# Optimization experiments

Measured on AMD Instinct MI355X. Metric: run time of the kernel, lower is better.

The kernel has to match this reference:

```python
import jax, jax.numpy as jnp
import numpy as np

N = 50000
NEG_SLOPE = 0.01  # F.leaky_relu default


def gcn_conv(x, edge_index, edge_weight, W, b):
    """PyG GCNConv: h = x @ W; symmetric-normalized aggregation with self-loops; + bias."""
    n = x.shape[0]
    h = x @ W                                # [N, out]
    src, dst = edge_index[0], edge_index[1]
    # degree includes self-loop weight 1.0 per node
    deg = jax.ops.segment_sum(edge_weight, dst, num_segments=n) + 1.0
    dinv = jax.lax.rsqrt(deg)                # deg >= 1, no zero guard needed
    norm = dinv[src] * edge_weight * dinv[dst]
    agg = jax.ops.segment_sum(norm[:, None] * h[src], dst, num_segments=n)
    agg = agg + (dinv * dinv)[:, None] * h   # self-loop contribution: deg^-1 * h_i
    return agg + b


def setup_inputs() -> dict:
    key = jax.random.key(0)
    ks = jax.random.split(key, 24)
    in_size, hid, out = 256, 64, 32
    E = 800000
    d = {}
    for i, nm in enumerate(["x1", "x2", "x3"]):
        d[nm] = jax.random.normal(ks[i], (N, in_size), dtype=jnp.float32)
    for i, nm in enumerate(["edge_index1", "edge_index2", "edge_index3"]):
        d[nm] = jax.random.randint(ks[3 + i], (2, E), 0, N, dtype=jnp.int32)
    for i, nm in enumerate(["edge_weight1", "edge_weight2", "edge_weight3"]):
        d[nm] = jax.random.uniform(ks[6 + i], (E,), dtype=jnp.float32)
    s_in = 1.0 / np.sqrt(in_size)
    s_h = 1.0 / np.sqrt(hid)
    for i, nm in enumerate(["W1", "W2", "W3"]):
        d[nm] = jax.random.uniform(ks[9 + i], (in_size, hid), minval=-s_in, maxval=s_in, dtype=jnp.float32)
    for i, nm in enumerate(["b1", "b2", "b3"]):
        d[nm] = jax.random.uniform(ks[12 + i], (hid,), minval=-s_in, maxval=s_in, dtype=jnp.float32)
    d["fc_w"] = jax.random.uniform(ks[15], (hid, 1), minval=-s_h, maxval=s_h, dtype=jnp.float32)
    d["fc_b"] = jax.random.uniform(ks[16], (1,), minval=-s_h, maxval=s_h, dtype=jnp.float32)
    for i, nm in enumerate(["W11", "W22", "W33"]):
        d[nm] = jax.random.uniform(ks[17 + i], (hid, out), minval=-s_h, maxval=s_h, dtype=jnp.float32)
    for i, nm in enumerate(["b11", "b22", "b33"]):
        d[nm] = jax.random.uniform(ks[20 + i], (out,), minval=-s_h, maxval=s_h, dtype=jnp.float32)
    return d


def reference(x1, x2, x3, edge_index1, edge_index2, edge_index3,
              edge_weight1, edge_weight2, edge_weight3,
              W1, W2, W3, b1, b2, b3, fc_w, fc_b,
              W11, W22, W33, b11, b22, b33):
    # branch embeddings (dropout is identity in eval mode)
    e1 = jax.nn.relu(gcn_conv(x1, edge_index1, edge_weight1, W1, b1))
    e2 = jax.nn.relu(gcn_conv(x2, edge_index2, edge_weight2, W2, b2))
    e3 = jax.nn.relu(gcn_conv(x3, edge_index3, edge_weight3, W3, b3))
    # attention coefficients
    c1 = jnp.exp(jax.nn.leaky_relu(e1 @ fc_w + fc_b, NEG_SLOPE))  # [N,1]
    c2 = jnp.exp(jax.nn.leaky_relu(e2 @ fc_w + fc_b, NEG_SLOPE))
    c3 = jnp.exp(jax.nn.leaky_relu(e3 @ fc_w + fc_b, NEG_SLOPE))
    cd = c1 + c2 + c3
    coef1, coef2, coef3 = c1 / cd, c2 / cd, c3 / cd
    combined = e1 * coef1 + e2 * coef2 + e3 * coef3
    out1 = gcn_conv(combined, edge_index1, edge_weight1, W11, b11)
    out2 = gcn_conv(combined, edge_index2, edge_weight2, W22, b22)
    out3 = gcn_conv(combined, edge_index3, edge_weight3, W33, b33)
    return (out1 + out2 + out3, coef1, coef2, coef3)
```

## Files before the change

kernel.cpp:

```cpp
#include <hip/hip_runtime.h>
#include <hip/hip_fp16.h>
#include <math.h>

#define NN    50000
#define INF_  256
#define HID   64
#define OUTF  32
#define EE    800000
#define TOTN  (3 * NN)
#define NBKT  196
#define NBIN  (3 * NBKT)
#define CBLK  392
#define NCNT  (3 * CBLK)
#define GB    782
#define NGEMM (3 * GB)
#define MAXB  5120
#define NBLK  12500

typedef unsigned long long u64;
typedef unsigned int       u32;
typedef unsigned short     u16;
typedef _Float16           f16;
typedef f16   f16x8 __attribute__((ext_vector_type(8)));
typedef f16   f16x4 __attribute__((ext_vector_type(4)));
typedef float f32x4 __attribute__((ext_vector_type(4)));

__global__ __launch_bounds__(256) void k_prep(
        const float* __restrict__ W1, const float* __restrict__ W2, const float* __restrict__ W3,
        f16* __restrict__ Wt2, u32* __restrict__ bin_total) {
    int blk = blockIdx.x, t = threadIdx.x;
    if (blk == 3) {
        for (int i = t; i < NBIN; i += 256) bin_total[i] = 0;
        return;
    }
    const float* W = (blk == 0) ? W1 : (blk == 1) ? W2 : W3;
    f16* wt = Wt2 + blk * 16384;
    for (int idx = t; idx < 16384; idx += 256) {
        int e    = idx & 7;
        int lane = (idx >> 3) & 63;
        int kt   = (idx >> 9) & 7;
        int c    = idx >> 12;
        int col  = c * 16 + (lane & 15);
        int k    = kt * 32 + ((lane >> 4) << 3) + e;
        wt[idx] = (f16)W[k * HID + col];
    }
}

__global__ __launch_bounds__(256) void k_count(
        const int* __restrict__ ei1, const int* __restrict__ ei2, const int* __restrict__ ei3,
        u32* __restrict__ bin_total, u32* __restrict__ blockbase) {
    __shared__ u32 bins[NBKT];
    int cb  = blockIdx.x;
    int br  = cb / CBLK;
    int blk = cb - br * CBLK;
    const int* ei = (br == 0) ? ei1 : (br == 1) ? ei2 : ei3;
    int t = threadIdx.x;
    for (int i = t; i < NBKT; i += 256) bins[i] = 0;
    __syncthreads();
    int e0 = blk * 2048;
#pragma unroll
    for (int k = 0; k < 8; ++k) {
        int e = e0 + k * 256 + t;
        if (e < EE) atomicAdd(&bins[(u32)ei[EE + e] >> 8], 1u);
    }
    __syncthreads();
    for (int i = t; i < NBKT; i += 256) {
        u32 c = bins[i];
        u32 base = atomicAdd(&bin_total[br * NBKT + i], c);
        blockbase[cb * NBKT + i] = base;
    }
}

__global__ __launch_bounds__(256) void k_scan(const u32* __restrict__ bin_total,
                                              u32* __restrict__ binstart) {
    __shared__ u32 s[256];
    int t = threadIdx.x;
    u32 c[3]; u32 sum = 0;
#pragma unroll
    for (int k = 0; k < 3; ++k) {
        int i = t * 3 + k;
        c[k] = (i < NBIN) ? bin_total[i] : 0;
        sum += c[k];
    }
    s[t] = sum;
    __syncthreads();
    for (int d = 1; d < 256; d <<= 1) {
        u32 v = (t >= d) ? s[t - d] : 0;
        __syncthreads();
        s[t] += v;
        __syncthreads();
    }
    u32 run = s[t] - sum;
#pragma unroll
    for (int k = 0; k < 3; ++k) {
        int i = t * 3 + k;
        if (i < NBIN) binstart[i] = run;
        run += c[k];
    }
    if (t == 255) binstart[NBIN] = run;
}

__global__ __launch_bounds__(256) void k_scatgemm(
        const int* __restrict__ ei1, const int* __restrict__ ei2, const int* __restrict__ ei3,
        const float* __restrict__ ew1, const float* __restrict__ ew2, const float* __restrict__ ew3,
        const u32* __restrict__ binstart, const u32* __restrict__ blockbase,
        u64* __restrict__ bucketed,
        const float* __restrict__ x1, const float* __restrict__ x2, const float* __restrict__ x3,
        const f16* __restrict__ Wt2, __half* __restrict__ h) {
    __shared__ f16 xl[64][264];
    int bid = blockIdx.x;
    int q = bid / 3, r = bid - q * 3;
    int t = threadIdx.x;

    if (r == 2) {
        u32* cur = (u32*)xl;
        int cb  = q;
        int br  = cb / CBLK;
        int blk = cb - br * CBLK;
        const int*   ei = (br == 0) ? ei1 : (br == 1) ? ei2 : ei3;
        const float* ew = (br == 0) ? ew1 : (br == 1) ? ew2 : ew3;
        for (int i = t; i < NBKT; i += 256) cur[i] = 0;
        __syncthreads();
        int e0 = blk * 2048;
#pragma unroll
        for (int k = 0; k < 8; ++k) {
            int e = e0 + k * 256 + t;
            if (e < EE) {
                u32 dst = (u32)ei[EE + e];
                u32 src = (u32)ei[e];
                u32 bkt = dst >> 8;
                u32 rnk = atomicAdd(&cur[bkt], 1u);
                u32 pos = binstart[br * NBKT + bkt] + blockbase[cb * NBKT + bkt] + rnk;
                bucketed[pos] = ((u64)__float_as_uint(ew[e]) << 32) | (src << 8) | (dst & 0xffu);
            }
        }
        return;
    }

    int gid = q * 2 + r;
    if (gid >= NGEMM) return;
    int b = gid / GB;
    int row_base = (gid - b * GB) * 64;
    const float4* x4 = reinterpret_cast<const float4*>((b == 0) ? x1 : (b == 1) ? x2 : x3);
    const f16* wt2 = Wt2 + b * 16384;
    __half* hb = h + (size_t)b * NN * HID;

    float4 v[16];
#pragma unroll
    for (int j = 0; j < 16; ++j) {
        int flat = j * 256 + t;
        int gr = row_base + (flat >> 6);
        v[j] = (gr < NN) ? x4[(size_t)row_base * 64 + flat]
                         : make_float4(0.f, 0.f, 0.f, 0.f);
    }
#pragma unroll
    for (int j = 0; j < 16; ++j) {
        int flat = j * 256 + t;
        int rr = flat >> 6, c4 = flat & 63;
        f16x4 p = {(f16)v[j].x, (f16)v[j].y, (f16)v[j].z, (f16)v[j].w};
        *(f16x4*)&xl[rr][c4 * 4] = p;
    }
    __syncthreads();

    int w    = t >> 6;
    int lane = t & 63;
    int lrow = lane & 15;
    int lk   = (lane >> 4) * 8;
    int arow = (w << 4) + lrow;

    f32x4 acc[4] = {{0,0,0,0},{0,0,0,0},{0,0,0,0},{0,0,0,0}};
#pragma unroll
    for (int kt = 0; kt < 8; ++kt) {
        f16x8 af = *(const f16x8*)&xl[arow][kt * 32 + lk];
#pragma unroll
        for (int c = 0; c < 4; ++c) {
            f16x8 bf = *(const f16x8*)&wt2[((c * 8 + kt) * 64 + lane) * 8];
            acc[c] = __builtin_amdgcn_mfma_f32_16x16x32_f16(af, bf, acc[c], 0, 0, 0);
        }
    }
    int orow0 = row_base + (w << 4) + ((lane >> 4) << 2);
#pragma unroll
    for (int c = 0; c < 4; ++c) {
#pragma unroll
        for (int i = 0; i < 4; ++i) {
            int row = orow0 + i;
            if (row < NN) hb[(size_t)row * HID + c * 16 + lrow] = __float2half(acc[c][i]);
        }
    }
}

__global__ __launch_bounds__(256) void k_bucket(
        const u64* __restrict__ bucketed, const u32* __restrict__ bin_total,
        const u32* __restrict__ binstart,
        u32* __restrict__ nodeinfo, float* __restrict__ dinv,
        u32* __restrict__ csr, __half* __restrict__ h) {
    __shared__ u32   scnt[256];
    __shared__ float swsum[256];
    __shared__ u32   scur[256];
    __shared__ u32   sscan[256];
    __shared__ float sdiv[256];
    __shared__ u32   lcsr[MAXB];
    int bin = blockIdx.x;
    int br  = bin / NBKT;
    int bkt = bin - br * NBKT;
    int t = threadIdx.x;
    u32 base = binstart[bin];
    u32 ecnt = bin_total[bin];
    scnt[t] = 0; swsum[t] = 0.f; scur[t] = 0;
    __syncthreads();
    for (u32 i = t; i < ecnt; i += 256) {
        u64 e = bucketed[base + i];
        u32 dl = (u32)e & 0xffu;
        atomicAdd(&scnt[dl], 1u);
        atomicAdd(&swsum[dl], __uint_as_float((u32)(e >> 32)));
    }
    __syncthreads();
    sscan[t] = scnt[t];
    __syncthreads();
    for (int d = 1; d < 256; d <<= 1) {
        u32 v = (t >= d) ? sscan[t - d] : 0;
        __syncthreads();
        sscan[t] += v;
        __syncthreads();
    }
    u32 lstart = sscan[t] - scnt[t];
    float d = rsqrtf(1.0f + swsum[t]);
    sdiv[t] = d;
    int n = bkt * 256 + t;
    if (n < NN) {
        int gi = br * NN + n;
        nodeinfo[gi] = ((base + lstart) << 10) | scnt[t];
        dinv[gi]     = d;
    }
    __syncthreads();
    for (u32 i = t; i < ecnt; i += 256) {
        u64 e = bucketed[base + i];
        u32 dl  = (u32)e & 0xffu;
        u32 src = (u32)(e >> 8) & 0xffffu;
        float w = __uint_as_float((u32)(e >> 32));
        u32 rnk = atomicAdd(&scur[dl], 1u);
        u32 ls  = sscan[dl] - scnt[dl];
        lcsr[ls + rnk] = ((u32)__half_as_ushort(__float2half(w)) << 16) | src;
    }
    __syncthreads();
    for (u32 i = t; i < ecnt; i += 256) csr[base + i] = lcsr[i];

    int nrows = NN - bkt * 256; if (nrows > 256) nrows = 256;
    u32* hrow = (u32*)(h + ((size_t)br * NN + (size_t)bkt * 256) * HID);
    for (int i = t; i < nrows * 32; i += 256) {
        float dd = sdiv[i >> 5];
        __half2 hv = *(__half2*)&hrow[i];
        float2 v = __half22float2(hv);
        __half2 r = __float22half2_rn(make_float2(v.x * dd, v.y * dd));
        hrow[i] = *(u32*)&r;
    }
}

__global__ __launch_bounds__(256) void k_agg1(
        const u32* __restrict__ csr, const u32* __restrict__ nodeinfo,
        const float* __restrict__ dinv,
        const float* __restrict__ b1, const float* __restrict__ b2, const float* __restrict__ b3,
        const __half* __restrict__ h, __half* __restrict__ e) {
    int bid = blockIdx.x;
    int br  = bid / NBLK;
    int nb  = bid - br * NBLK;
    int t   = threadIdx.x;
    int f2  = t & 31;
    int eo  = (t >> 5) & 1;
    int sub = __builtin_amdgcn_readfirstlane(t >> 6);
    int n   = nb * 4 + sub;

    const float* bi = (br == 0) ? b1 : (br == 1) ? b2 : b3;
    const __half2* hb2 = (const __half2*)(h + (size_t)br * NN * HID);
    int i   = br * NN + n;
    u32 inf = nodeinfo[i];
    int cc  = (int)(inf & 1023u);
    int st  = (int)(inf >> 10);
    float d = dinv[i];
    float2 hs = __half22float2(hb2[(size_t)n * 32 + f2]);

    float ax = 0.f, ay = 0.f;
    int cm1 = cc - 1;
    for (int j = 0; j < cc; j += 16) {
        u32 ee[8]; __half2 vv[8];
#pragma unroll
        for (int u = 0; u < 8; ++u) {
            int jj = j + 2 * u + eo;
            ee[u] = csr[st + (jj < cm1 ? jj : cm1)];
            if (jj >= cc) ee[u] &= 0xffffu;
        }
#pragma unroll
        for (int u = 0; u < 8; ++u)
            vv[u] = hb2[(size_t)(ee[u] & 0xffff) * 32 + f2];
#pragma unroll
        for (int u = 0; u < 8; ++u) {
            float w = __half2float(__ushort_as_half((u16)(ee[u] >> 16)));
            float2 v = __half22float2(vv[u]);
            ax = fmaf(w, v.x, ax);
            ay = fmaf(w, v.y, ay);
        }
    }
    ax += __shfl_xor(ax, 32);
    ay += __shfl_xor(ay, 32);
    float2 bv = ((const float2*)bi)[f2];
    float ex = fmaxf(bv.x + d * (hs.x + ax), 0.f);
    float ey = fmaxf(bv.y + d * (hs.y + ay), 0.f);
    if (eo == 0)
        ((__half2*)e)[((size_t)br * NN + n) * 32 + f2] = __float22half2_rn(make_float2(ex, ey));
}

__global__ __launch_bounds__(256) void k_attn(
        const __half* __restrict__ e,
        const float* __restrict__ fc_w, const float* __restrict__ fc_b,
        __half* __restrict__ comb, float* __restrict__ coef_out) {
    int t    = threadIdx.x;
    int lane = t & 63;
    int sub  = __builtin_amdgcn_readfirstlane(t >> 6);
    int half = lane >> 5;
    int f2   = lane & 31;
    int n    = blockIdx.x * 8 + sub * 2 + half;
    float2 wv = ((const float2*)fc_w)[f2];
    float fb = fc_b[0];
    const __half2* e2 = (const __half2*)e;

    float2 ev[3]; float c[3];
#pragma unroll
    for (int b = 0; b < 3; ++b) {
        ev[b] = __half22float2(e2[((size_t)b * NN + n) * 32 + f2]);
        float dd = ev[b].x * wv.x + ev[b].y * wv.y;
#pragma unroll
        for (int off = 16; off > 0; off >>= 1) dd += __shfl_xor(dd, off);
        float z = dd + fb;
        z = (z > 0.f) ? z : 0.01f * z;
        c[b] = expf(z);
    }
    float cd = c[0] + c[1] + c[2];
    float coef0 = c[0] / cd, coef1 = c[1] / cd, coef2 = c[2] / cd;
    float cx = ev[0].x * coef0 + ev[1].x * coef1 + ev[2].x * coef2;
    float cy = ev[0].y * coef0 + ev[1].y * coef1 + ev[2].y * coef2;
    ((__half2*)comb)[(size_t)n * 32 + f2] = __float22half2_rn(make_float2(cx, cy));
    if (f2 == 0) {
        coef_out[n]          = coef0;
        coef_out[NN + n]     = coef1;
        coef_out[2 * NN + n] = coef2;
    }
}

__global__ __launch_bounds__(256) void k_gemm2(
        const __half* __restrict__ comb,
        const float* __restrict__ W11, const float* __restrict__ W22, const float* __restrict__ W33,
        const float* __restrict__ dinv, __half* __restrict__ h2) {
    __shared__ float Wls[3][HID][OUTF];
    __shared__ __half cl[8][HID];
    int t = threadIdx.x;
    {
        const float4* w40 = reinterpret_cast<const float4*>(W11);
        const float4* w41 = reinterpret_cast<const float4*>(W22);
        const float4* w42 = reinterpret_cast<const float4*>(W33);
        float4* d0 = reinterpret_cast<float4*>(&Wls[0][0][0]);
        float4* d1 = reinterpret_cast<float4*>(&Wls[1][0][0]);
        float4* d2 = reinterpret_cast<float4*>(&Wls[2][0][0]);
#pragma unroll
        for (int j = 0; j < 2; ++j) {
            d0[t + j * 256] = w40[t + j * 256];
            d1[t + j * 256] = w41[t + j * 256];
            d2[t + j * 256] = w42[t + j * 256];
        }
    }
    int row0 = blockIdx.x * 8;
    ((u32*)cl)[t] = ((const u32*)(comb + (size_t)row0 * HID))[t];
    __syncthreads();

    int col = t & 31;
    int rr  = t >> 5;
    int row = row0 + rr;
    float a0 = 0.f, a1 = 0.f, a2 = 0.f;
    for (int k = 0; k < HID; ++k) {
        float cv = __half2float(cl[rr][k]);
        a0 = fmaf(cv, Wls[0][k][col], a0);
        a1 = fmaf(cv, Wls[1][k][col], a1);
        a2 = fmaf(cv, Wls[2][k][col], a2);
    }
    float d0 = dinv[row], d1 = dinv[NN + row], d2 = dinv[2 * NN + row];
    h2[(size_t)0 * NN * OUTF + (size_t)row * OUTF + col] = __float2half(a0 * d0);
    h2[(size_t)1 * NN * OUTF + (size_t)row * OUTF + col] = __float2half(a1 * d1);
    h2[(size_t)2 * NN * OUTF + (size_t)row * OUTF + col] = __float2half(a2 * d2);
}

__global__ __launch_bounds__(256) void k_agg2p(
        const u32* __restrict__ csr, const u32* __restrict__ nodeinfo,
        const float* __restrict__ dinv,
        const __half* __restrict__ h2, float* __restrict__ outp) {
    int bid = blockIdx.x;
    int br  = bid / NBLK;
    int nb  = bid - br * NBLK;
    int t   = threadIdx.x;
    int f2  = t & 15;
    int eo  = (t >> 4) & 3;
    int sub = __builtin_amdgcn_readfirstlane(t >> 6);
    int n   = nb * 4 + sub;

    int i   = br * NN + n;
    u32 inf = nodeinfo[i];
    int cc  = (int)(inf & 1023u);
    int st  = (int)(inf >> 10);
    const __half2* h2b = (const __half2*)(h2 + (size_t)br * NN * OUTF);
    float ax = 0.f, ay = 0.f;
    int cm1 = cc - 1;
    for (int j = 0; j < cc; j += 16) {
        u32 ee[4]; __half2 vv[4];
#pragma unroll
        for (int u = 0; u < 4; ++u) {
            int jj = j + 4 * u + eo;
            ee[u] = csr[st + (jj < cm1 ? jj : cm1)];
            if (jj >= cc) ee[u] &= 0xffffu;
        }
#pragma unroll
        for (int u = 0; u < 4; ++u)
            vv[u] = h2b[(size_t)(ee[u] & 0xffff) * 16 + f2];
#pragma unroll
        for (int u = 0; u < 4; ++u) {
            float w = __half2float(__ushort_as_half((u16)(ee[u] >> 16)));
            float2 v = __half22float2(vv[u]);
            ax = fmaf(w, v.x, ax);
            ay = fmaf(w, v.y, ay);
        }
    }
    ax += __shfl_xor(ax, 16); ay += __shfl_xor(ay, 16);
    ax += __shfl_xor(ax, 32); ay += __shfl_xor(ay, 32);
    float d = dinv[i];
    float2 hs = __half22float2(h2b[(size_t)n * 16 + f2]);
    if (eo == 0)
        ((float2*)outp)[((size_t)br * NN + n) * 16 + f2] =
            make_float2(d * (ax + hs.x), d * (ay + hs.y));
}

__global__ __launch_bounds__(256) void k_sum(
        const float* __restrict__ outp,
        const float* __restrict__ b11, const float* __restrict__ b22, const float* __restrict__ b33,
        float* __restrict__ out) {
    int i = blockIdx.x * 256 + threadIdx.x;
    int f2 = i & 15;
    const float2* p = (const float2*)outp;
    float2 v0 = p[i];
    float2 v1 = p[(size_t)NN * 16 + i];
    float2 v2 = p[(size_t)2 * NN * 16 + i];
    float2 bA = ((const float2*)b11)[f2];
    float2 bB = ((const float2*)b22)[f2];
    float2 bC = ((const float2*)b33)[f2];
    ((float2*)out)[i] = make_float2(v0.x + v1.x + v2.x + bA.x + bB.x + bC.x,
                                    v0.y + v1.y + v2.y + bA.y + bB.y + bC.y);
}

extern "C" void kernel_launch(void* const* d_in, const int* in_sizes, int n_in,
                              void* d_out, int out_size, void* d_ws, size_t ws_size,
                              hipStream_t stream) {
    const float* x1  = (const float*)d_in[0];
    const float* x2  = (const float*)d_in[1];
    const float* x3  = (const float*)d_in[2];
    const int*   ei1 = (const int*)d_in[3];
    const int*   ei2 = (const int*)d_in[4];
    const int*   ei3 = (const int*)d_in[5];
    const float* ew1 = (const float*)d_in[6];
    const float* ew2 = (const float*)d_in[7];
    const float* ew3 = (const float*)d_in[8];
    const float* W1  = (const float*)d_in[9];
    const float* W2  = (const float*)d_in[10];
    const float* W3  = (const float*)d_in[11];
    const float* b1  = (const float*)d_in[12];
    const float* b2  = (const float*)d_in[13];
    const float* b3  = (const float*)d_in[14];
    const float* fcw = (const float*)d_in[15];
    const float* fcb = (const float*)d_in[16];
    const float* W11 = (const float*)d_in[17];
    const float* W22 = (const float*)d_in[18];
    const float* W33 = (const float*)d_in[19];
    const float* b11 = (const float*)d_in[20];
    const float* b22 = (const float*)d_in[21];
    const float* b33 = (const float*)d_in[22];

    float* out = (float*)d_out;
    float* coef_out = out + (size_t)NN * OUTF;

    u64*   bucketed  = (u64*)d_ws;
    float* outp      = (float*)d_ws;
    u32*   csr       = (u32*)(bucketed + 3 * EE);
    u32*   bin_total = csr + 3 * EE;
    u32*   binstart  = bin_total + NBIN;
    u32*   blockbase = binstart + NBIN + 4;
    float* dinv      = (float*)(blockbase + NCNT * NBKT);
    u32*   nodeinfo  = (u32*)(dinv + TOTN);
    f16*   Wt2       = (f16*)(nodeinfo + TOTN);
    __half* h        = (__half*)(Wt2 + 3 * 16384);
    __half* comb     = h + (size_t)TOTN * HID;
    __half* h2       = comb + (size_t)NN * HID;
    __half* e        = h2 + (size_t)TOTN * OUTF;

    k_prep<<<dim3(4), 256, 0, stream>>>(W1, W2, W3, Wt2, bin_total);
    k_count<<<dim3(NCNT), 256, 0, stream>>>(ei1, ei2, ei3, bin_total, blockbase);
    k_scan<<<dim3(1), 256, 0, stream>>>(bin_total, binstart);
    k_scatgemm<<<dim3(NCNT * 3), 256, 0, stream>>>(ei1, ei2, ei3, ew1, ew2, ew3,
                                                   binstart, blockbase, bucketed,
                                                   x1, x2, x3, Wt2, h);
    k_bucket<<<dim3(NBIN), 256, 0, stream>>>(bucketed, bin_total, binstart,
                                             nodeinfo, dinv, csr, h);

    k_agg1<<<dim3(3 * NBLK), 256, 0, stream>>>(csr, nodeinfo, dinv, b1, b2, b3, h, e);
    k_attn<<<dim3(NN / 8), 256, 0, stream>>>(e, fcw, fcb, comb, coef_out);
    k_gemm2<<<dim3(NN / 8), 256, 0, stream>>>(comb, W11, W22, W33, dinv, h2);
    k_agg2p<<<dim3(3 * NBLK), 256, 0, stream>>>(csr, nodeinfo, dinv, h2, outp);
    k_sum<<<dim3(3125), 256, 0, stream>>>(outp, b11, b22, b33, out);
}
```

Baseline: 286.5 us.

## Stage edge scatter in shared memory for coalesced bucketed writes, larger edge chunks

The edge-scatter blocks now first count and prefix-scan destination buckets locally, place each edge into a shared-memory staging array sorted by bucket, and then write that array to global memory in contiguous runs instead of doing random 8-byte scattered stores. Edge chunks grow from 2048 to 4096 per block, which halves the count/scatter block count, and the kernel's block mix changes to four GEMM blocks per scatter block. Edge weights are converted to fp16 at scatter time, so the bucket kernel no longer converts them. The cost is an extra pass over edge indices, a 256-step shared scan, and a larger shared footprint that may reduce occupancy.

```diff
diff --git a/kernel.cpp b/kernel.cpp
--- a/kernel.cpp
+++ b/kernel.cpp
@@ -10,7 +10,7 @@
 #define TOTN  (3 * NN)
 #define NBKT  196
 #define NBIN  (3 * NBKT)
-#define CBLK  392
+#define CBLK  196
 #define NCNT  (3 * CBLK)
 #define GB    782
 #define NGEMM (3 * GB)
@@ -20,6 +20,7 @@
 typedef unsigned long long u64;
 typedef unsigned int       u32;
 typedef unsigned short     u16;
+typedef unsigned char      u8;
 typedef _Float16           f16;
 typedef f16   f16x8 __attribute__((ext_vector_type(8)));
 typedef f16   f16x4 __attribute__((ext_vector_type(4)));
@@ -57,9 +58,9 @@
     int t = threadIdx.x;
     for (int i = t; i < NBKT; i += 256) bins[i] = 0;
     __syncthreads();
-    int e0 = blk * 2048;
-#pragma unroll
-    for (int k = 0; k < 8; ++k) {
+    int e0 = blk * 4096;
+#pragma unroll
+    for (int k = 0; k < 16; ++k) {
         int e = e0 + k * 256 + t;
         if (e < EE) atomicAdd(&bins[(u32)ei[EE + e] >> 8], 1u);
     }
@@ -107,38 +108,70 @@
         u64* __restrict__ bucketed,
         const float* __restrict__ x1, const float* __restrict__ x2, const float* __restrict__ x3,
         const f16* __restrict__ Wt2, __half* __restrict__ h) {
-    __shared__ f16 xl[64][264];
+    __shared__ __align__(16) char smem[36864];
     int bid = blockIdx.x;
-    int q = bid / 3, r = bid - q * 3;
+    int q = bid / 5, r = bid - q * 5;
     int t = threadIdx.x;
 
-    if (r == 2) {
-        u32* cur = (u32*)xl;
+    if (r == 4) {
+        u64* ent  = (u64*)smem;
+        u32* acnt = (u32*)(smem + 32768);
+        u32* ascn = acnt + 256;
+        u32* acur = ascn + 256;
+        u32* adel = acur + 256;
         int cb  = q;
         int br  = cb / CBLK;
         int blk = cb - br * CBLK;
         const int*   ei = (br == 0) ? ei1 : (br == 1) ? ei2 : ei3;
         const float* ew = (br == 0) ? ew1 : (br == 1) ? ew2 : ew3;
-        for (int i = t; i < NBKT; i += 256) cur[i] = 0;
-        __syncthreads();
-        int e0 = blk * 2048;
-#pragma unroll
-        for (int k = 0; k < 8; ++k) {
+        acnt[t] = 0; acur[t] = 0;
+        __syncthreads();
+        int e0 = blk * 4096;
+        int tot = EE - e0; if (tot > 4096) tot = 4096;
+#pragma unroll
+        for (int k = 0; k < 16; ++k) {
+            int e = e0 + k * 256 + t;
+            if (e < EE) atomicAdd(&acnt[(u32)ei[EE + e] >> 8], 1u);
+        }
+        __syncthreads();
+        ascn[t] = acnt[t];
+        __syncthreads();
+        for (int d = 1; d < 256; d <<= 1) {
+            u32 v = (t >= d) ? ascn[t - d] : 0;
+            __syncthreads();
+            ascn[t] += v;
+            __syncthreads();
+        }
+        if (t < NBKT)
+            adel[t] = binstart[br * NBKT + t] + blockbase[cb * NBKT + t]
+                      - (ascn[t] - acnt[t]);
+        __syncthreads();
+#pragma unroll
+        for (int k = 0; k < 16; ++k) {
             int e = e0 + k * 256 + t;
             if (e < EE) {
                 u32 dst = (u32)ei[EE + e];
                 u32 src = (u32)ei[e];
                 u32 bkt = dst >> 8;
-                u32 rnk = atomicAdd(&cur[bkt], 1u);
-                u32 pos = binstart[br * NBKT + bkt] + blockbase[cb * NBKT + bkt] + rnk;
-                bucketed[pos] = ((u64)__float_as_uint(ew[e]) << 32) | (src << 8) | (dst & 0xffu);
+                u16 w16 = __half_as_ushort(__float2half(ew[e]));
+                u32 rnk = atomicAdd(&acur[bkt], 1u);
+                u32 ls  = ascn[bkt] - acnt[bkt] + rnk;
+                ent[ls] = ((u64)bkt << 48) | ((u64)w16 << 32)
+                        | ((u64)src << 8) | (u64)(dst & 0xffu);
             }
         }
+        __syncthreads();
+        for (int i = t; i < tot; i += 256) {
+            u64 ev = ent[i];
+            u32 bkt = (u32)(ev >> 48) & 0xffu;
+            bucketed[adel[bkt] + i] = ev;
+        }
         return;
     }
 
-    int gid = q * 2 + r;
+    int gid = q * 4 + r;
     if (gid >= NGEMM) return;
+    f16 (*xl)[264] = reinterpret_cast<f16(*)[264]>(smem);
     int b = gid / GB;
     int row_base = (gid - b * GB) * 64;
     const float4* x4 = reinterpret_cast<const float4*>((b == 0) ? x1 : (b == 1) ? x2 : x3);
@@ -212,7 +245,7 @@
         u64 e = bucketed[base + i];
         u32 dl = (u32)e & 0xffu;
         atomicAdd(&scnt[dl], 1u);
-        atomicAdd(&swsum[dl], __uint_as_float((u32)(e >> 32)));
+        atomicAdd(&swsum[dl], __half2float(__ushort_as_half((u16)((e >> 32) & 0xffffu))));
     }
     __syncthreads();
     sscan[t] = scnt[t];
@@ -237,10 +270,10 @@
         u64 e = bucketed[base + i];
         u32 dl  = (u32)e & 0xffu;
         u32 src = (u32)(e >> 8) & 0xffffu;
-        float w = __uint_as_float((u32)(e >> 32));
+        u32 w16 = (u32)(e >> 32) & 0xffffu;
         u32 rnk = atomicAdd(&scur[dl], 1u);
         u32 ls  = sscan[dl] - scnt[dl];
-        lcsr[ls + rnk] = ((u32)__half_as_ushort(__float2half(w)) << 16) | src;
+        lcsr[ls + rnk] = (w16 << 16) | src;
     }
     __syncthreads();
     for (u32 i = t; i < ecnt; i += 256) csr[base + i] = lcsr[i];
@@ -251,8 +284,8 @@
         float dd = sdiv[i >> 5];
         __half2 hv = *(__half2*)&hrow[i];
         float2 v = __half22float2(hv);
-        __half2 r = __float22half2_rn(make_float2(v.x * dd, v.y * dd));
-        hrow[i] = *(u32*)&r;
+        __half2 rr = __float22half2_rn(make_float2(v.x * dd, v.y * dd));
+        hrow[i] = *(u32*)&rr;
     }
 }
 
@@ -499,7 +532,7 @@
     k_prep<<<dim3(4), 256, 0, stream>>>(W1, W2, W3, Wt2, bin_total);
     k_count<<<dim3(NCNT), 256, 0, stream>>>(ei1, ei2, ei3, bin_total, blockbase);
     k_scan<<<dim3(1), 256, 0, stream>>>(bin_total, binstart);
-    k_scatgemm<<<dim3(NCNT * 3), 256, 0, stream>>>(ei1, ei2, ei3, ew1, ew2, ew3,
+    k_scatgemm<<<dim3(NCNT * 5), 256, 0, stream>>>(ei1, ei2, ei3, ew1, ew2, ew3,
                                                    binstart, blockbase, bucketed,
                                                    x1, x2, x3, Wt2, h);
     k_bucket<<<dim3(NBIN), 256, 0, stream>>>(bucketed, bin_total, binstart,
```

Result: faster. 272.5 us (-4.9%).
